# Kernel tuning notes

Hardware: AMD Instinct MI355X
Metric: run time of the kernel (lower is better)

Reference implementation:

```python
import jax, jax.numpy as jnp
import numpy as np

B, S, E = 16, 2048, 1024

def setup_inputs() -> dict:
    key = jax.random.key(0)
    ks = jax.random.split(key, 7)
    scale = 1.0 / np.sqrt(E)
    x = jax.random.normal(ks[0], (B, S, E), dtype=jnp.float32)
    wq = jax.random.normal(ks[1], (E, E), dtype=jnp.float32) * scale
    bq = jax.random.normal(ks[2], (E,), dtype=jnp.float32) * 0.01
    wk = jax.random.normal(ks[3], (E, E), dtype=jnp.float32) * scale
    bk = jax.random.normal(ks[4], (E,), dtype=jnp.float32) * 0.01
    wv = jax.random.normal(ks[5], (E, E), dtype=jnp.float32) * scale
    bv = jax.random.normal(ks[6], (E,), dtype=jnp.float32) * 0.01
    return {"x": x, "wq": wq, "bq": bq, "wk": wk, "bk": bk, "wv": wv, "bv": bv}

def reference(x, wq, bq, wk, bk, wv, bv):
    # Linear layers: y = x @ W^T + b (torch nn.Linear convention)
    Q = jnp.einsum('bse,fe->bsf', x, wq) + bq
    K = jnp.einsum('bse,fe->bsf', x, wk) + bk
    V = jnp.einsum('bse,fe->bsf', x, wv) + bv
    scale = 1.0 / jnp.sqrt(jnp.asarray(x.shape[-1], dtype=x.dtype))
    score = jnp.einsum('bqe,bke->bqk', Q, K) * scale  # [B,S,S]
    attn = jax.nn.softmax(score, axis=-1)
    # dropout is identity in eval mode
    context = jnp.einsum('bqk,bke->bqe', attn, V)  # [B,S,E]
    return jnp.mean(context, axis=1)  # [B,E]
```

## Files before the change

### kernel.cpp

```cpp
#include <hip/hip_runtime.h>


#define B_ 16
#define S_ 2048
#define E_ 1024

typedef __bf16 bf16x8 __attribute__((ext_vector_type(8)));
typedef float f32x4 __attribute__((ext_vector_type(4)));
typedef float f32x2 __attribute__((ext_vector_type(2)));

__device__ __forceinline__ unsigned short f2bf(float f) {
  unsigned int u = __float_as_uint(f);
  u = (u + 0x7FFFu + ((u >> 16) & 1u)) >> 16;
  return (unsigned short)u;
}

__global__ __launch_bounds__(256) void gvec_kernel(
    const float* __restrict__ wk, const float* __restrict__ bq,
    float* __restrict__ g) {
  const int e = blockIdx.x * 256 + threadIdx.x;
  const int f0 = blockIdx.y * 32;
  float acc = 0.f;
#pragma unroll
  for (int i = 0; i < 32; ++i) acc += wk[(size_t)(f0 + i) * E_ + e] * bq[f0 + i];
  atomicAdd(&g[e], acc);
}

__global__ __launch_bounds__(256) void cast_x_v_kernel(
    const float* __restrict__ x, const float* __restrict__ g,
    unsigned short* __restrict__ xbf, float* __restrict__ vs) {
  const int row = blockIdx.x, t = threadIdx.x;
  const size_t i = (size_t)row * E_ + t * 4;
  float4 v = *(const float4*)(x + i);
  float4 gv = *(const float4*)(g + t * 4);
  ushort4 o;
  o.x = f2bf(v.x); o.y = f2bf(v.y); o.z = f2bf(v.z); o.w = f2bf(v.w);
  *(ushort4*)(xbf + i) = o;
  float p = v.x * gv.x + v.y * gv.y + v.z * gv.z + v.w * gv.w;
#pragma unroll
  for (int off = 32; off >= 1; off >>= 1) p += __shfl_xor(p, off);
  __shared__ float wsp[4];
  if ((t & 63) == 0) wsp[t >> 6] = p;
  __syncthreads();
  if (t == 0) vs[row] = (wsp[0] + wsp[1] + wsp[2] + wsp[3]) * 0.03125f;
}

__global__ __launch_bounds__(256) void tcast_kernel(
    const float* __restrict__ src, unsigned short* __restrict__ dst) {
  __shared__ float tile[32][33];
  const int tx = threadIdx.x & 31, ty = threadIdx.x >> 5;
  const int f0 = blockIdx.y * 32, e0 = blockIdx.x * 32;
#pragma unroll
  for (int j = 0; j < 4; ++j)
    tile[ty + 8 * j][tx] = src[(size_t)(f0 + ty + 8 * j) * E_ + e0 + tx];
  __syncthreads();
#pragma unroll
  for (int j = 0; j < 4; ++j)
    dst[(size_t)(e0 + ty + 8 * j) * E_ + f0 + tx] = f2bf(tile[tx][ty + 8 * j]);
}

template <int MODE>
__global__ __launch_bounds__(256, 2) void gemm_bt(
    const unsigned short* __restrict__ A, const unsigned short* __restrict__ Bm,
    void* __restrict__ Cout, const float* __restrict__ bias,
    float* __restrict__ rowsum, float scale,
    int K, int lda, int ldb, int ldc,
    long long strideA, long long strideB, long long strideC) {
  __shared__ unsigned short As[128 * 64];
  __shared__ unsigned short Bs[128 * 64];

  const int tid = threadIdx.x;
  const int wave = tid >> 6;
  const int lane = tid & 63;
  const int bz = blockIdx.z;
  const unsigned short* Ab = A + (size_t)bz * strideA;
  const unsigned short* Bb = Bm + (size_t)bz * strideB;
  const int rowBase = blockIdx.y * 128;
  const int colBase = blockIdx.x * 128;

  const int waveM = wave >> 1, waveN = wave & 1;
  const int lrow = lane & 15, lq = lane >> 4;

  const int rsub = lane >> 3;
  const int gOff = (((lane & 7) ^ rsub) << 3);

  f32x4 acc[4][4];
#pragma unroll
  for (int i = 0; i < 4; ++i)
#pragma unroll
    for (int j = 0; j < 4; ++j) {
      f32x4 z = {0.f, 0.f, 0.f, 0.f};
      acc[i][j] = z;
    }

  for (int k0 = 0; k0 < K; k0 += 64) {
#pragma unroll
    for (int i = 0; i < 4; ++i) {
      const int chunk = wave * 4 + i;
      const int r = chunk * 8 + rsub;
      const unsigned short* ga = Ab + (size_t)(rowBase + r) * lda + (k0 + gOff);
      const unsigned short* gb = Bb + (size_t)(colBase + r) * ldb + (k0 + gOff);
      __builtin_amdgcn_global_load_lds(
          (const __attribute__((address_space(1))) void*)ga,
          (__attribute__((address_space(3))) void*)(&As[chunk * 512]), 16, 0, 0);
      __builtin_amdgcn_global_load_lds(
          (const __attribute__((address_space(1))) void*)gb,
          (__attribute__((address_space(3))) void*)(&Bs[chunk * 512]), 16, 0, 0);
    }
    __syncthreads();

#pragma unroll
    for (int ks = 0; ks < 2; ++ks) {
      const int gg = (((ks * 4 + lq) ^ (lrow & 7)) << 3);
      bf16x8 af[4], bfv[4];
#pragma unroll
      for (int mi = 0; mi < 4; ++mi)
        af[mi] = *(const bf16x8*)(&As[(waveM * 64 + mi * 16 + lrow) * 64 + gg]);
#pragma unroll
      for (int ni = 0; ni < 4; ++ni)
        bfv[ni] = *(const bf16x8*)(&Bs[(waveN * 64 + ni * 16 + lrow) * 64 + gg]);
#pragma unroll
      for (int mi = 0; mi < 4; ++mi)
#pragma unroll
        for (int ni = 0; ni < 4; ++ni)
          acc[mi][ni] = __builtin_amdgcn_mfma_f32_16x16x32_bf16(
              af[mi], bfv[ni], acc[mi][ni], 0, 0, 0);
    }
    __syncthreads();
  }

  if constexpr (MODE == 0) {
    unsigned short* Cb = (unsigned short*)Cout + (size_t)bz * strideC;
#pragma unroll
    for (int mi = 0; mi < 4; ++mi) {
      const int grow = rowBase + waveM * 64 + mi * 16 + lq * 4;
#pragma unroll
      for (int ni = 0; ni < 4; ++ni) {
        const int gcol = colBase + waveN * 64 + ni * 16 + lrow;
        const float badd = bias ? bias[gcol] : 0.f;
#pragma unroll
        for (int r = 0; r < 4; ++r)
          Cb[(size_t)(grow + r) * ldc + gcol] =
              f2bf(acc[mi][ni][r] * scale + badd);
      }
    }
  } else {
    unsigned char* Eb = (unsigned char*)Cout + (size_t)bz * strideC;
    float* rs = rowsum + (size_t)bz * S_;
    const float* vsb = bias + (size_t)bz * S_;
    float badd[4];
#pragma unroll
    for (int ni = 0; ni < 4; ++ni)
      badd[ni] = vsb[colBase + waveN * 64 + ni * 16 + lrow];
#pragma unroll
    for (int mi = 0; mi < 4; ++mi) {
      const int grow = rowBase + waveM * 64 + mi * 16 + lq * 4;
#pragma unroll
      for (int r = 0; r < 4; ++r) {
        float e[4];
        float partial = 0.f;
#pragma unroll
        for (int ni = 0; ni < 4; ++ni) {
          e[ni] = __expf(acc[mi][ni][r] * scale + badd[ni]);
          partial += e[ni];
        }
        unsigned int pk = 0;
        pk = __builtin_amdgcn_cvt_pk_fp8_f32(e[0], e[1], pk, false);
        pk = __builtin_amdgcn_cvt_pk_fp8_f32(e[2], e[3], pk, true);
        *(unsigned int*)(&Eb[(size_t)(grow + r) * S_ + colBase + waveN * 64 +
                             lrow * 4]) = pk;
        partial += __shfl_xor(partial, 1);
        partial += __shfl_xor(partial, 2);
        partial += __shfl_xor(partial, 4);
        partial += __shfl_xor(partial, 8);
        if (lrow == 0) atomicAdd(&rs[grow + r], partial);
      }
    }
  }
}

__global__ __launch_bounds__(256) void colsum_kernel(
    const unsigned int* __restrict__ Epk, const float* __restrict__ rowsum,
    float* __restrict__ wsum) {
  const int b = blockIdx.y, q0 = blockIdx.x * 64, t = threadIdx.x;
  __shared__ float rinv[64];
  if (t < 64) rinv[t] = 1.0f / rowsum[(size_t)b * S_ + q0 + t];
  __syncthreads();
  float cs[2][4] = {{0, 0, 0, 0}, {0, 0, 0, 0}};
  const unsigned int* Eb = Epk + ((size_t)b * S_ + q0) * (S_ / 4);
  for (int q = 0; q < 64; ++q) {
    const float rv = rinv[q];
    const unsigned int* row = Eb + (size_t)q * (S_ / 4);
#pragma unroll
    for (int j = 0; j < 2; ++j) {
      const unsigned int p = row[t + 256 * j];
      f32x2 lo = __builtin_amdgcn_cvt_pk_f32_fp8(p, false);
      f32x2 hi = __builtin_amdgcn_cvt_pk_f32_fp8(p, true);
      cs[j][0] += lo[0] * rv;
      cs[j][1] += lo[1] * rv;
      cs[j][2] += hi[0] * rv;
      cs[j][3] += hi[1] * rv;
    }
  }
  const float inv = 1.0f / (float)S_;
#pragma unroll
  for (int j = 0; j < 2; ++j) {
    const int d = t + 256 * j;
    const int base = (d >> 4) * 64 + (d & 15);
#pragma unroll
    for (int jj = 0; jj < 4; ++jj)
      atomicAdd(&wsum[(size_t)b * S_ + base + 16 * jj], cs[j][jj] * inv);
  }
}

__global__ __launch_bounds__(256) void xbar_kernel(
    const float* __restrict__ x, const float* __restrict__ wsum,
    float* __restrict__ xbar) {
  const int b = blockIdx.y, kc = blockIdx.x, t = threadIdx.x;
  float4 acc = {0.f, 0.f, 0.f, 0.f};
  for (int k0 = 0; k0 < 128; ++k0) {
    const int k = kc * 128 + k0;
    const float w = wsum[(size_t)b * S_ + k];
    const float4 xv = *(const float4*)(x + ((size_t)b * S_ + k) * E_ + t * 4);
    acc.x += w * xv.x; acc.y += w * xv.y;
    acc.z += w * xv.z; acc.w += w * xv.w;
  }
  float* xb = xbar + (size_t)b * E_ + t * 4;
  atomicAdd(&xb[0], acc.x);
  atomicAdd(&xb[1], acc.y);
  atomicAdd(&xb[2], acc.z);
  atomicAdd(&xb[3], acc.w);
}

__global__ __launch_bounds__(256) void out_kernel(
    const float* __restrict__ xbar, const float* __restrict__ wv,
    const float* __restrict__ bv, float* __restrict__ out) {
  const int gid = blockIdx.x * 256 + threadIdx.x;
  const int b = gid >> 10, e = gid & 1023;
  const int c0 = blockIdx.y * 64;
  const float4* xr = (const float4*)(xbar + (size_t)b * E_) + c0;
  const float4* wr = (const float4*)(wv + (size_t)e * E_) + c0;
  float s = 0.f;
  for (int j = 0; j < 64; ++j) {
    float4 a = xr[j], w = wr[j];
    s += a.x * w.x + a.y * w.y + a.z * w.z + a.w * w.w;
  }
  if (blockIdx.y == 0) s += bv[e];
  atomicAdd(&out[gid], s);
}

extern "C" void kernel_launch(void* const* d_in, const int* in_sizes, int n_in,
                              void* d_out, int out_size, void* d_ws,
                              size_t ws_size, hipStream_t stream) {
  const float* x = (const float*)d_in[0];
  const float* wq = (const float*)d_in[1];
  const float* bq = (const float*)d_in[2];
  const float* wk = (const float*)d_in[3];
  const float* wv = (const float*)d_in[5];
  const float* bv = (const float*)d_in[6];
  float* out = (float*)d_out;

  char* ws = (char*)d_ws;
  const size_t MB = 1ull << 20;
  unsigned short* xbf = (unsigned short*)(ws);
  unsigned short* y = (unsigned short*)(ws + 64 * MB);
  unsigned char* Ebuf = (unsigned char*)(ws + 128 * MB);
  unsigned short* WqT = (unsigned short*)(ws + 192 * MB);
  unsigned short* WkT = (unsigned short*)(ws + 194 * MB);
  unsigned short* Mt = (unsigned short*)(ws + 196 * MB);
  float* g = (float*)(ws + 198 * MB);
  float* rowsum = g + E_;
  float* wsum = rowsum + B_ * S_;
  float* xbar = wsum + B_ * S_;
  float* vs = xbar + B_ * E_;

  hipMemsetAsync(g, 0, (size_t)(E_ + 2 * B_ * S_ + B_ * E_) * sizeof(float),
                 stream);
  hipMemsetAsync(out, 0, (size_t)B_ * E_ * sizeof(float), stream);

  gvec_kernel<<<dim3(E_ / 256, 32), 256, 0, stream>>>(wk, bq, g);
  cast_x_v_kernel<<<B_ * S_, 256, 0, stream>>>(x, g, xbf, vs);
  tcast_kernel<<<dim3(32, 32), 256, 0, stream>>>(wq, WqT);
  tcast_kernel<<<dim3(32, 32), 256, 0, stream>>>(wk, WkT);

  gemm_bt<0><<<dim3(8, 8), 256, 0, stream>>>(
      WkT, WqT, (void*)Mt, nullptr, nullptr, 1.0f, E_, E_, E_, E_, 0, 0, 0);
  gemm_bt<0><<<dim3(E_ / 128, (B_ * S_) / 128), 256, 0, stream>>>(
      xbf, Mt, (void*)y, nullptr, nullptr, 1.0f, E_, E_, E_, E_, 0, 0, 0);
  gemm_bt<1><<<dim3(S_ / 128, S_ / 128, B_), 256, 0, stream>>>(
      y, xbf, (void*)Ebuf, vs, rowsum, 0.03125f, E_, E_, E_, S_,
      (long long)S_ * E_, (long long)S_ * E_, (long long)S_ * S_);

  colsum_kernel<<<dim3(S_ / 64, B_), 256, 0, stream>>>(
      (const unsigned int*)Ebuf, rowsum, wsum);
  xbar_kernel<<<dim3(16, B_), 256, 0, stream>>>(x, wsum, xbar);
  out_kernel<<<dim3(B_ * E_ / 256, 4), 256, 0, stream>>>(xbar, wv, bv, out);
}
```

Baseline: 512.0 us.

## Run score GEMM in FP8 with MX-scaled MFMA and emit FP8 intermediates

The big batched score GEMM (y·x^T, 16×2048×2048×1024) now takes FP8 (e4m3) operands and uses the 16x16x128 scaled MFMA with unit scales, in place of the bf16 16x16x32 MFMA. The y GEMM writes FP8 output packed in the permuted order the new kernel expects, and the x cast kernel also writes a matching FP8 copy of x. xbar now reads the bf16 x instead of fp32 x, halving that read. This aims to double matrix throughput and halve operand traffic for the dominant GEMM, at the cost of much lower precision in the attention scores before exp.

```diff
diff --git a/kernel.cpp b/kernel.cpp
--- a/kernel.cpp
+++ b/kernel.cpp
@@ -8,6 +8,7 @@
 typedef __bf16 bf16x8 __attribute__((ext_vector_type(8)));
 typedef float f32x4 __attribute__((ext_vector_type(4)));
 typedef float f32x2 __attribute__((ext_vector_type(2)));
+typedef int i32x8 __attribute__((ext_vector_type(8)));
 
 __device__ __forceinline__ unsigned short f2bf(float f) {
   unsigned int u = __float_as_uint(f);
@@ -28,7 +29,8 @@
 
 __global__ __launch_bounds__(256) void cast_x_v_kernel(
     const float* __restrict__ x, const float* __restrict__ g,
-    unsigned short* __restrict__ xbf, float* __restrict__ vs) {
+    unsigned short* __restrict__ xbf, unsigned int* __restrict__ xf8,
+    float* __restrict__ vs) {
   const int row = blockIdx.x, t = threadIdx.x;
   const size_t i = (size_t)row * E_ + t * 4;
   float4 v = *(const float4*)(x + i);
@@ -36,6 +38,14 @@
   ushort4 o;
   o.x = f2bf(v.x); o.y = f2bf(v.y); o.z = f2bf(v.z); o.w = f2bf(v.w);
   *(ushort4*)(xbf + i) = o;
+  {
+    const int grp = t >> 4, lr = t & 15;
+    const float* xr = x + (size_t)row * E_ + grp * 64 + lr;
+    unsigned int pk = 0;
+    pk = __builtin_amdgcn_cvt_pk_fp8_f32(xr[0], xr[16], pk, false);
+    pk = __builtin_amdgcn_cvt_pk_fp8_f32(xr[32], xr[48], pk, true);
+    xf8[(size_t)row * (E_ / 4) + t] = pk;
+  }
   float p = v.x * gv.x + v.y * gv.y + v.z * gv.z + v.w * gv.w;
 #pragma unroll
   for (int off = 32; off >= 1; off >>= 1) p += __shfl_xor(p, off);
@@ -62,25 +72,13 @@
 template <int MODE>
 __global__ __launch_bounds__(256, 2) void gemm_bt(
     const unsigned short* __restrict__ A, const unsigned short* __restrict__ Bm,
-    void* __restrict__ Cout, const float* __restrict__ bias,
-    float* __restrict__ rowsum, float scale,
-    int K, int lda, int ldb, int ldc,
-    long long strideA, long long strideB, long long strideC) {
+    void* __restrict__ Cout, int K, int lda, int ldb, int ldc) {
   __shared__ unsigned short As[128 * 64];
   __shared__ unsigned short Bs[128 * 64];
-
-  const int tid = threadIdx.x;
-  const int wave = tid >> 6;
-  const int lane = tid & 63;
-  const int bz = blockIdx.z;
-  const unsigned short* Ab = A + (size_t)bz * strideA;
-  const unsigned short* Bb = Bm + (size_t)bz * strideB;
-  const int rowBase = blockIdx.y * 128;
-  const int colBase = blockIdx.x * 128;
-
+  const int tid = threadIdx.x, wave = tid >> 6, lane = tid & 63;
+  const int rowBase = blockIdx.y * 128, colBase = blockIdx.x * 128;
   const int waveM = wave >> 1, waveN = wave & 1;
   const int lrow = lane & 15, lq = lane >> 4;
-
   const int rsub = lane >> 3;
   const int gOff = (((lane & 7) ^ rsub) << 3);
 
@@ -98,8 +96,8 @@
     for (int i = 0; i < 4; ++i) {
       const int chunk = wave * 4 + i;
       const int r = chunk * 8 + rsub;
-      const unsigned short* ga = Ab + (size_t)(rowBase + r) * lda + (k0 + gOff);
-      const unsigned short* gb = Bb + (size_t)(colBase + r) * ldb + (k0 + gOff);
+      const unsigned short* ga = A + (size_t)(rowBase + r) * lda + (k0 + gOff);
+      const unsigned short* gb = Bm + (size_t)(colBase + r) * ldb + (k0 + gOff);
       __builtin_amdgcn_global_load_lds(
           (const __attribute__((address_space(1))) void*)ga,
           (__attribute__((address_space(3))) void*)(&As[chunk * 512]), 16, 0, 0);
@@ -108,7 +106,6 @@
           (__attribute__((address_space(3))) void*)(&Bs[chunk * 512]), 16, 0, 0);
     }
     __syncthreads();
-
 #pragma unroll
     for (int ks = 0; ks < 2; ++ks) {
       const int gg = (((ks * 4 + lq) ^ (lrow & 7)) << 3);
@@ -130,51 +127,138 @@
   }
 
   if constexpr (MODE == 0) {
-    unsigned short* Cb = (unsigned short*)Cout + (size_t)bz * strideC;
+    unsigned short* Cb = (unsigned short*)Cout;
 #pragma unroll
     for (int mi = 0; mi < 4; ++mi) {
       const int grow = rowBase + waveM * 64 + mi * 16 + lq * 4;
 #pragma unroll
       for (int ni = 0; ni < 4; ++ni) {
         const int gcol = colBase + waveN * 64 + ni * 16 + lrow;
-        const float badd = bias ? bias[gcol] : 0.f;
 #pragma unroll
         for (int r = 0; r < 4; ++r)
-          Cb[(size_t)(grow + r) * ldc + gcol] =
-              f2bf(acc[mi][ni][r] * scale + badd);
+          Cb[(size_t)(grow + r) * ldc + gcol] = f2bf(acc[mi][ni][r]);
       }
     }
   } else {
-    unsigned char* Eb = (unsigned char*)Cout + (size_t)bz * strideC;
-    float* rs = rowsum + (size_t)bz * S_;
-    const float* vsb = bias + (size_t)bz * S_;
-    float badd[4];
-#pragma unroll
-    for (int ni = 0; ni < 4; ++ni)
-      badd[ni] = vsb[colBase + waveN * 64 + ni * 16 + lrow];
+    unsigned int* Cd = (unsigned int*)Cout;
+    const int dbase = (colBase + waveN * 64) >> 2;
 #pragma unroll
     for (int mi = 0; mi < 4; ++mi) {
       const int grow = rowBase + waveM * 64 + mi * 16 + lq * 4;
 #pragma unroll
       for (int r = 0; r < 4; ++r) {
-        float e[4];
-        float partial = 0.f;
-#pragma unroll
-        for (int ni = 0; ni < 4; ++ni) {
-          e[ni] = __expf(acc[mi][ni][r] * scale + badd[ni]);
-          partial += e[ni];
-        }
         unsigned int pk = 0;
-        pk = __builtin_amdgcn_cvt_pk_fp8_f32(e[0], e[1], pk, false);
-        pk = __builtin_amdgcn_cvt_pk_fp8_f32(e[2], e[3], pk, true);
-        *(unsigned int*)(&Eb[(size_t)(grow + r) * S_ + colBase + waveN * 64 +
-                             lrow * 4]) = pk;
-        partial += __shfl_xor(partial, 1);
-        partial += __shfl_xor(partial, 2);
-        partial += __shfl_xor(partial, 4);
-        partial += __shfl_xor(partial, 8);
-        if (lrow == 0) atomicAdd(&rs[grow + r], partial);
+        pk = __builtin_amdgcn_cvt_pk_fp8_f32(acc[mi][0][r], acc[mi][1][r], pk,
+                                             false);
+        pk = __builtin_amdgcn_cvt_pk_fp8_f32(acc[mi][2][r], acc[mi][3][r], pk,
+                                             true);
+        Cd[(size_t)(grow + r) * (ldc >> 2) + dbase + lrow] = pk;
       }
+    }
+  }
+}
+
+__global__ __launch_bounds__(256, 2) void gemm_mx_exp(
+    const unsigned char* __restrict__ A, const unsigned char* __restrict__ Bm,
+    unsigned char* __restrict__ Eout, const float* __restrict__ vs,
+    float* __restrict__ rowsum, float scale) {
+  __shared__ __align__(16) unsigned char As[128 * 128];
+  __shared__ __align__(16) unsigned char Bs[128 * 128];
+  const int tid = threadIdx.x, wave = tid >> 6, lane = tid & 63;
+  const int bz = blockIdx.z;
+  const unsigned char* Ab = A + (size_t)bz * S_ * E_;
+  const unsigned char* Bb = Bm + (size_t)bz * S_ * E_;
+  const int rowBase = blockIdx.y * 128, colBase = blockIdx.x * 128;
+  const int waveM = wave >> 1, waveN = wave & 1;
+  const int lrow = lane & 15, quad = lane >> 4;
+  const int rsub = lane >> 3;
+  const int gOff = (((lane & 7) ^ rsub) << 4);
+
+  f32x4 acc[4][4];
+#pragma unroll
+  for (int i = 0; i < 4; ++i)
+#pragma unroll
+    for (int j = 0; j < 4; ++j) {
+      f32x4 z = {0.f, 0.f, 0.f, 0.f};
+      acc[i][j] = z;
+    }
+
+  const int p0 = ((2 * quad) ^ (lrow & 7)) << 4;
+  const int p1 = ((2 * quad + 1) ^ (lrow & 7)) << 4;
+
+  for (int k0 = 0; k0 < E_; k0 += 128) {
+#pragma unroll
+    for (int i = 0; i < 4; ++i) {
+      const int chunk = wave * 4 + i;
+      const int r = chunk * 8 + rsub;
+      const unsigned char* ga = Ab + (size_t)(rowBase + r) * E_ + k0 + gOff;
+      const unsigned char* gb = Bb + (size_t)(colBase + r) * E_ + k0 + gOff;
+      __builtin_amdgcn_global_load_lds(
+          (const __attribute__((address_space(1))) void*)ga,
+          (__attribute__((address_space(3))) void*)(&As[chunk * 1024]), 16, 0,
+          0);
+      __builtin_amdgcn_global_load_lds(
+          (const __attribute__((address_space(1))) void*)gb,
+          (__attribute__((address_space(3))) void*)(&Bs[chunk * 1024]), 16, 0,
+          0);
+    }
+    __syncthreads();
+
+    i32x8 af[4], bfv[4];
+#pragma unroll
+    for (int mi = 0; mi < 4; ++mi) {
+      const int r = waveM * 64 + mi * 16 + lrow;
+      int4 lo = *(const int4*)(&As[r * 128 + p0]);
+      int4 hi = *(const int4*)(&As[r * 128 + p1]);
+      i32x8 f = {lo.x, lo.y, lo.z, lo.w, hi.x, hi.y, hi.z, hi.w};
+      af[mi] = f;
+    }
+#pragma unroll
+    for (int ni = 0; ni < 4; ++ni) {
+      const int r = waveN * 64 + ni * 16 + lrow;
+      int4 lo = *(const int4*)(&Bs[r * 128 + p0]);
+      int4 hi = *(const int4*)(&Bs[r * 128 + p1]);
+      i32x8 f = {lo.x, lo.y, lo.z, lo.w, hi.x, hi.y, hi.z, hi.w};
+      bfv[ni] = f;
+    }
+#pragma unroll
+    for (int mi = 0; mi < 4; ++mi)
+#pragma unroll
+      for (int ni = 0; ni < 4; ++ni)
+        acc[mi][ni] = __builtin_amdgcn_mfma_scale_f32_16x16x128_f8f6f4(
+            af[mi], bfv[ni], acc[mi][ni], 0, 0, 0, 0x7F7F7F7F, 0, 0x7F7F7F7F);
+    __syncthreads();
+  }
+
+  unsigned char* Eb = Eout + (size_t)bz * S_ * S_;
+  float* rs = rowsum + (size_t)bz * S_;
+  const float* vsb = vs + (size_t)bz * S_;
+  float badd[4];
+#pragma unroll
+  for (int ni = 0; ni < 4; ++ni)
+    badd[ni] = vsb[colBase + waveN * 64 + ni * 16 + lrow];
+#pragma unroll
+  for (int mi = 0; mi < 4; ++mi) {
+    const int grow = rowBase + waveM * 64 + mi * 16 + quad * 4;
+#pragma unroll
+    for (int r = 0; r < 4; ++r) {
+      float e[4];
+      float partial = 0.f;
+#pragma unroll
+      for (int ni = 0; ni < 4; ++ni) {
+        e[ni] = __expf(acc[mi][ni][r] * scale + badd[ni]);
+        partial += e[ni];
+      }
+      unsigned int pk = 0;
+      pk = __builtin_amdgcn_cvt_pk_fp8_f32(e[0], e[1], pk, false);
+      pk = __builtin_amdgcn_cvt_pk_fp8_f32(e[2], e[3], pk, true);
+      *(unsigned int*)(&Eb[(size_t)(grow + r) * S_ + colBase + waveN * 64 +
+                           lrow * 4]) = pk;
+      partial += __shfl_xor(partial, 1);
+      partial += __shfl_xor(partial, 2);
+      partial += __shfl_xor(partial, 4);
+      partial += __shfl_xor(partial, 8);
+      if (lrow == 0) atomicAdd(&rs[grow + r], partial);
     }
   }
 }
@@ -214,16 +298,19 @@
 }
 
 __global__ __launch_bounds__(256) void xbar_kernel(
-    const float* __restrict__ x, const float* __restrict__ wsum,
+    const unsigned short* __restrict__ xbf, const float* __restrict__ wsum,
     float* __restrict__ xbar) {
   const int b = blockIdx.y, kc = blockIdx.x, t = threadIdx.x;
   float4 acc = {0.f, 0.f, 0.f, 0.f};
   for (int k0 = 0; k0 < 128; ++k0) {
     const int k = kc * 128 + k0;
     const float w = wsum[(size_t)b * S_ + k];
-    const float4 xv = *(const float4*)(x + ((size_t)b * S_ + k) * E_ + t * 4);
-    acc.x += w * xv.x; acc.y += w * xv.y;
-    acc.z += w * xv.z; acc.w += w * xv.w;
+    const ushort4 xv =
+        *(const ushort4*)(xbf + ((size_t)b * S_ + k) * E_ + t * 4);
+    acc.x += w * __uint_as_float((unsigned int)xv.x << 16);
+    acc.y += w * __uint_as_float((unsigned int)xv.y << 16);
+    acc.z += w * __uint_as_float((unsigned int)xv.z << 16);
+    acc.w += w * __uint_as_float((unsigned int)xv.w << 16);
   }
   float* xb = xbar + (size_t)b * E_ + t * 4;
   atomicAdd(&xb[0], acc.x);
@@ -263,8 +350,9 @@
   char* ws = (char*)d_ws;
   const size_t MB = 1ull << 20;
   unsigned short* xbf = (unsigned short*)(ws);
-  unsigned short* y = (unsigned short*)(ws + 64 * MB);
-  unsigned char* Ebuf = (unsigned char*)(ws + 128 * MB);
+  unsigned char* yf8 = (unsigned char*)(ws + 64 * MB);
+  unsigned char* Ebuf = (unsigned char*)(ws + 96 * MB);
+  unsigned int* xf8 = (unsigned int*)(ws + 160 * MB);
   unsigned short* WqT = (unsigned short*)(ws + 192 * MB);
   unsigned short* WkT = (unsigned short*)(ws + 194 * MB);
   unsigned short* Mt = (unsigned short*)(ws + 196 * MB);
@@ -279,20 +367,19 @@
   hipMemsetAsync(out, 0, (size_t)B_ * E_ * sizeof(float), stream);
 
   gvec_kernel<<<dim3(E_ / 256, 32), 256, 0, stream>>>(wk, bq, g);
-  cast_x_v_kernel<<<B_ * S_, 256, 0, stream>>>(x, g, xbf, vs);
+  cast_x_v_kernel<<<B_ * S_, 256, 0, stream>>>(x, g, xbf, xf8, vs);
   tcast_kernel<<<dim3(32, 32), 256, 0, stream>>>(wq, WqT);
   tcast_kernel<<<dim3(32, 32), 256, 0, stream>>>(wk, WkT);
 
-  gemm_bt<0><<<dim3(8, 8), 256, 0, stream>>>(
-      WkT, WqT, (void*)Mt, nullptr, nullptr, 1.0f, E_, E_, E_, E_, 0, 0, 0);
-  gemm_bt<0><<<dim3(E_ / 128, (B_ * S_) / 128), 256, 0, stream>>>(
-      xbf, Mt, (void*)y, nullptr, nullptr, 1.0f, E_, E_, E_, E_, 0, 0, 0);
-  gemm_bt<1><<<dim3(S_ / 128, S_ / 128, B_), 256, 0, stream>>>(
-      y, xbf, (void*)Ebuf, vs, rowsum, 0.03125f, E_, E_, E_, S_,
-      (long long)S_ * E_, (long long)S_ * E_, (long long)S_ * S_);
+  gemm_bt<0><<<dim3(8, 8), 256, 0, stream>>>(WkT, WqT, (void*)Mt, E_, E_, E_,
+                                             E_);
+  gemm_bt<2><<<dim3(E_ / 128, (B_ * S_) / 128), 256, 0, stream>>>(
+      xbf, Mt, (void*)yf8, E_, E_, E_, E_);
+  gemm_mx_exp<<<dim3(S_ / 128, S_ / 128, B_), 256, 0, stream>>>(
+      yf8, (const unsigned char*)xf8, Ebuf, vs, rowsum, 0.03125f);
 
   colsum_kernel<<<dim3(S_ / 64, B_), 256, 0, stream>>>(
       (const unsigned int*)Ebuf, rowsum, wsum);
-  xbar_kernel<<<dim3(16, B_), 256, 0, stream>>>(x, wsum, xbar);
+  xbar_kernel<<<dim3(16, B_), 256, 0, stream>>>(xbf, wsum, xbar);
   out_kernel<<<dim3(B_ * E_ / 256, 4), 256, 0, stream>>>(xbar, wv, bv, out);
 }
```

New measurement: 862.4 us. +68.4%, slower.
